# Optimization experiments

Measured on AMD Instinct MI355X. Metric: run time of the kernel, lower is better.

The kernel has to match this reference:

```python
import jax, jax.numpy as jnp
import numpy as np

D_MODEL = 1024
N_HEADS = 16
TOP_FACTOR = 5


def setup_inputs() -> dict:
    key = jax.random.key(0)
    ks = jax.random.split(key, 9)
    B, L, D = 2, 4096, D_MODEL
    s = 0.02
    return {
        "x": jax.random.normal(ks[0], (B, L, D), dtype=jnp.float32),
        "Wq": jax.random.normal(ks[1], (D, D), dtype=jnp.float32) * s,
        "bq": jnp.zeros((D,), dtype=jnp.float32),
        "Wk": jax.random.normal(ks[2], (D, D), dtype=jnp.float32) * s,
        "bk": jnp.zeros((D,), dtype=jnp.float32),
        "Wv": jax.random.normal(ks[3], (D, D), dtype=jnp.float32) * s,
        "bv": jnp.zeros((D,), dtype=jnp.float32),
        "Wo": jax.random.normal(ks[4], (D, D), dtype=jnp.float32) * s,
        "bo": jnp.zeros((D,), dtype=jnp.float32),
    }


def reference(x, Wq, bq, Wk, bk, Wv, bv, Wo, bo):
    B, L, D = x.shape
    H = N_HEADS
    hd = D // H
    BH = B * H
    top_u = max(1, L // TOP_FACTOR)

    def proj(W, b):
        # [B,L,D] -> [B*H, L, hd] (matches view + transpose(1,2) in torch)
        y = x @ W.T + b
        return y.reshape(B, L, H, hd).transpose(0, 2, 1, 3).reshape(BH, L, hd)

    Q = proj(Wq, bq)
    K = proj(Wk, bk)
    V = proj(Wv, bv)

    # select top-u queries per (batch,head) by L2 norm
    query_norms = jnp.linalg.norm(Q, axis=2)              # [BH, L]
    _, top_idx = jax.lax.top_k(query_norms, top_u)        # [BH, top_u]
    Q_sel = jnp.take_along_axis(Q, top_idx[:, :, None], axis=1)  # [BH, u, hd]

    scale = 1.0 / (hd ** 0.5)
    scores = jnp.einsum('bud,bld->bul', Q_sel, K) * scale  # [BH, u, L]
    attn = jax.nn.softmax(scores, axis=-1)
    out_sel = jnp.einsum('bul,bld->bud', attn, V)          # [BH, u, hd]

    # scatter selected outputs back; non-selected rows stay zero
    out_full = jnp.zeros((BH, L, hd), dtype=x.dtype)
    out_full = out_full.at[jnp.arange(BH)[:, None], top_idx].set(out_sel)

    out = out_full.reshape(B, H, L, hd).transpose(0, 2, 1, 3).reshape(B, L, D)
    return out @ Wo.T + bo
```

## Files before the change

kernel.cpp:

```cpp
#include <hip/hip_runtime.h>
#include <cstddef>
#include <cstdint>

constexpr int LSEQ = 4096;
constexpr int DM   = 1024;
constexpr int HD   = 64;
constexpr int BHT  = 32;
constexpr int TOPU = 819;
constexpr int MROWS = 8192;

typedef unsigned short u16;
typedef __attribute__((ext_vector_type(8))) short short8v;
typedef __attribute__((ext_vector_type(4))) short short4v;
typedef __attribute__((ext_vector_type(4))) float f32x4;

__device__ __forceinline__ u16 f2bf(float f) {
  uint32_t u = __float_as_uint(f);
  u += 0x7fffu + ((u >> 16) & 1u);
  return (u16)(u >> 16);
}
__device__ __forceinline__ float bf2f(u16 h) {
  return __uint_as_float(((uint32_t)h) << 16);
}

__device__ __forceinline__ void gl16(const void* g, void* l) {
  __builtin_amdgcn_global_load_lds(
      (const __attribute__((address_space(1))) void*)g,
      (__attribute__((address_space(3))) void*)l, 16, 0, 0);
}

__device__ __forceinline__ void inv_swz(int S, int& R, int& C) {
  const int R0 = ((S >> 5) ^ (S >> 7)) & 1;
  const int R1 = (S >> 6) & 1;
  R = ((S >> 6) << 1) | R0;
  C = (((S >> 3) & 1) ^ R0) | ((((S >> 4) & 1) ^ R1) << 1);
}

__device__ __forceinline__ void split3_body(const float* src, u16* p1, u16* p2,
                                            u16* p3, int i) {
  const float4 a = *reinterpret_cast<const float4*>(src + (size_t)i * 8);
  const float4 b = *reinterpret_cast<const float4*>(src + (size_t)i * 8 + 4);
  float e[8] = {a.x, a.y, a.z, a.w, b.x, b.y, b.z, b.w};
  short8v v1, v2, v3;
  #pragma unroll
  for (int j = 0; j < 8; ++j) {
    u16 h1 = f2bf(e[j]);        float r1 = e[j] - bf2f(h1);
    u16 h2 = f2bf(r1);          float r2 = r1 - bf2f(h2);
    u16 h3 = f2bf(r2);
    v1[j] = (short)h1; v2[j] = (short)h2; v3[j] = (short)h3;
  }
  *reinterpret_cast<short8v*>(p1 + (size_t)i * 8) = v1;
  *reinterpret_cast<short8v*>(p2 + (size_t)i * 8) = v2;
  *reinterpret_cast<short8v*>(p3 + (size_t)i * 8) = v3;
}

__device__ __forceinline__ void conv_body(const float* src, u16* dst, int i) {
  const float4 a = *reinterpret_cast<const float4*>(src + (size_t)i * 8);
  const float4 b = *reinterpret_cast<const float4*>(src + (size_t)i * 8 + 4);
  short8v v;
  v[0] = (short)f2bf(a.x); v[1] = (short)f2bf(a.y);
  v[2] = (short)f2bf(a.z); v[3] = (short)f2bf(a.w);
  v[4] = (short)f2bf(b.x); v[5] = (short)f2bf(b.y);
  v[6] = (short)f2bf(b.z); v[7] = (short)f2bf(b.w);
  *reinterpret_cast<short8v*>(dst + (size_t)i * 8) = v;
}

__global__ __launch_bounds__(256) void prep_all(
    const float* __restrict__ x,  const float* __restrict__ Wq,
    const float* __restrict__ Wk, const float* __restrict__ Wv,
    const float* __restrict__ Wo,
    u16* __restrict__ x1, u16* __restrict__ x2, u16* __restrict__ x3,
    u16* __restrict__ wq1, u16* __restrict__ wq2, u16* __restrict__ wq3,
    u16* __restrict__ Wkb, u16* __restrict__ Wvb, u16* __restrict__ Wob)
{
  const int NX = MROWS * DM / 8;
  const int NW = DM * DM / 8;
  int i = blockIdx.x * 256 + threadIdx.x;
  if (i < NX)                { split3_body(x,  x1,  x2,  x3,  i); return; }
  i -= NX;
  if (i < NW)                { split3_body(Wq, wq1, wq2, wq3, i); return; }
  i -= NW;
  if (i < NW)                { conv_body(Wk, Wkb, i); return; }
  i -= NW;
  if (i < NW)                { conv_body(Wv, Wvb, i); return; }
  i -= NW;
  if (i < NW)                { conv_body(Wo, Wob, i); }
}

__global__ __launch_bounds__(256) void gemm_q_split(
    const u16* __restrict__ X1, const u16* __restrict__ X2, const u16* __restrict__ X3,
    const u16* __restrict__ W1, const u16* __restrict__ W2, const u16* __restrict__ W3,
    const float* __restrict__ bias, float* __restrict__ Y,
    float* __restrict__ norms)
{
  __shared__ u16 As[3][128 * 32];
  __shared__ u16 Bs[3][128 * 32];
  const int tid = threadIdx.x;
  const int m0 = blockIdx.x * 128, n0 = blockIdx.y * 128;
  const int wid = tid >> 6, lane = tid & 63;
  const int wr = (wid >> 1) * 64, wc = (wid & 1) * 64;
  const int c = lane & 15, G = lane >> 4;

  int Rr[2], Cr[2];
  #pragma unroll
  for (int rr = 0; rr < 2; ++rr) inv_swz((tid + rr * 256) * 8, Rr[rr], Cr[rr]);

  f32x4 acc[4][4];
  #pragma unroll
  for (int mt = 0; mt < 4; ++mt)
    #pragma unroll
    for (int nt = 0; nt < 4; ++nt)
      acc[mt][nt] = (f32x4){0.f, 0.f, 0.f, 0.f};

  for (int k0 = 0; k0 < DM; k0 += 32) {
    #pragma unroll
    for (int rr = 0; rr < 2; ++rr) {
      const size_t goA = (size_t)(m0 + Rr[rr]) * DM + k0 + Cr[rr] * 8;
      const size_t goB = (size_t)(n0 + Rr[rr]) * DM + k0 + Cr[rr] * 8;
      const int lb = wid * 512 + rr * 2048;
      gl16(X1 + goA, &As[0][lb]);
      gl16(X2 + goA, &As[1][lb]);
      gl16(X3 + goA, &As[2][lb]);
      gl16(W1 + goB, &Bs[0][lb]);
      gl16(W2 + goB, &Bs[1][lb]);
      gl16(W3 + goB, &Bs[2][lb]);
    }
    __syncthreads();

    short8v bf[3][4];
    #pragma unroll
    for (int nt = 0; nt < 4; ++nt) {
      const int n = wc + nt * 16 + c;
      const int eo = (n * 32 + G * 8) ^ ((n & 7) << 3);
      bf[0][nt] = *reinterpret_cast<const short8v*>(&Bs[0][eo]);
      bf[1][nt] = *reinterpret_cast<const short8v*>(&Bs[1][eo]);
      bf[2][nt] = *reinterpret_cast<const short8v*>(&Bs[2][eo]);
    }
    #pragma unroll
    for (int mt = 0; mt < 4; ++mt) {
      const int m = wr + mt * 16 + c;
      const int eo = (m * 32 + G * 8) ^ ((m & 7) << 3);
      short8v a1 = *reinterpret_cast<const short8v*>(&As[0][eo]);
      short8v a2 = *reinterpret_cast<const short8v*>(&As[1][eo]);
      short8v a3 = *reinterpret_cast<const short8v*>(&As[2][eo]);
      #pragma unroll
      for (int nt = 0; nt < 4; ++nt) {
        acc[mt][nt] = __builtin_amdgcn_mfma_f32_16x16x32_bf16(a1, bf[0][nt], acc[mt][nt], 0, 0, 0);
        acc[mt][nt] = __builtin_amdgcn_mfma_f32_16x16x32_bf16(a1, bf[1][nt], acc[mt][nt], 0, 0, 0);
        acc[mt][nt] = __builtin_amdgcn_mfma_f32_16x16x32_bf16(a2, bf[0][nt], acc[mt][nt], 0, 0, 0);
        acc[mt][nt] = __builtin_amdgcn_mfma_f32_16x16x32_bf16(a2, bf[1][nt], acc[mt][nt], 0, 0, 0);
        acc[mt][nt] = __builtin_amdgcn_mfma_f32_16x16x32_bf16(a1, bf[2][nt], acc[mt][nt], 0, 0, 0);
        acc[mt][nt] = __builtin_amdgcn_mfma_f32_16x16x32_bf16(a3, bf[0][nt], acc[mt][nt], 0, 0, 0);
      }
    }
    __syncthreads();
  }

  float bb[4];
  #pragma unroll
  for (int nt = 0; nt < 4; ++nt) bb[nt] = bias[n0 + wc + nt * 16 + c];

  float ns[4][4];
  #pragma unroll
  for (int mt = 0; mt < 4; ++mt)
    #pragma unroll
    for (int r = 0; r < 4; ++r) ns[mt][r] = 0.f;

  #pragma unroll
  for (int mt = 0; mt < 4; ++mt) {
    #pragma unroll
    for (int nt = 0; nt < 4; ++nt) {
      const int n = n0 + wc + nt * 16 + c;
      const int h = n >> 6, d = n & 63;
      #pragma unroll
      for (int r = 0; r < 4; ++r) {
        const int m = m0 + wr + mt * 16 + G * 4 + r;
        const int b = m >> 12, l = m & (LSEQ - 1);
        const float val = acc[mt][nt][r] + bb[nt];
        Y[((size_t)((b << 4) + h) * LSEQ + l) * HD + d] = val;
        ns[mt][r] = fmaf(val, val, ns[mt][r]);
      }
    }
  }
  #pragma unroll
  for (int mt = 0; mt < 4; ++mt)
    #pragma unroll
    for (int r = 0; r < 4; ++r) {
      float v = ns[mt][r];
      v += __shfl_xor(v, 1); v += __shfl_xor(v, 2);
      v += __shfl_xor(v, 4); v += __shfl_xor(v, 8);
      ns[mt][r] = v;
    }
  if (c == 0) {
    const int h = (n0 + wc) >> 6;
    #pragma unroll
    for (int mt = 0; mt < 4; ++mt)
      #pragma unroll
      for (int r = 0; r < 4; ++r) {
        const int m = m0 + wr + mt * 16 + G * 4 + r;
        const int b = m >> 12, l = m & (LSEQ - 1);
        norms[(((size_t)((b << 4) + h)) << 12) + l] = ns[mt][r];
      }
  }
}

__global__ __launch_bounds__(256) void gemm_kv(
    const u16* __restrict__ Xb, const u16* __restrict__ Wkb, const u16* __restrict__ Wvb,
    const float* __restrict__ bkp, const float* __restrict__ bvp,
    u16* __restrict__ Kb, u16* __restrict__ VgT)
{
  __shared__ u16 smem[128 * 136];
  u16* As = smem;
  u16* Bs = smem + 4096;
  const int tid = threadIdx.x;
  const bool isV = blockIdx.y >= 8;
  const int m0 = blockIdx.x * 128, n0 = (blockIdx.y & 7) * 128;
  const u16* Wb = isV ? Wvb : Wkb;
  const float* bias = isV ? bvp : bkp;
  const int wid = tid >> 6, lane = tid & 63;
  const int wr = (wid >> 1) * 64, wc = (wid & 1) * 64;
  const int c = lane & 15, G = lane >> 4;

  int Rr[2], Cr[2];
  #pragma unroll
  for (int rr = 0; rr < 2; ++rr) inv_swz((tid + rr * 256) * 8, Rr[rr], Cr[rr]);

  f32x4 acc[4][4];
  #pragma unroll
  for (int mt = 0; mt < 4; ++mt)
    #pragma unroll
    for (int nt = 0; nt < 4; ++nt)
      acc[mt][nt] = (f32x4){0.f, 0.f, 0.f, 0.f};

  for (int k0 = 0; k0 < DM; k0 += 32) {
    #pragma unroll
    for (int rr = 0; rr < 2; ++rr) {
      const size_t goA = (size_t)(m0 + Rr[rr]) * DM + k0 + Cr[rr] * 8;
      const size_t goB = (size_t)(n0 + Rr[rr]) * DM + k0 + Cr[rr] * 8;
      const int lb = wid * 512 + rr * 2048;
      gl16(Xb + goA, As + lb);
      gl16(Wb + goB, Bs + lb);
    }
    __syncthreads();

    short8v af[4], bf[4];
    #pragma unroll
    for (int mt = 0; mt < 4; ++mt) {
      const int m = wr + mt * 16 + c;
      af[mt] = *reinterpret_cast<const short8v*>(As + ((m * 32 + G * 8) ^ ((m & 7) << 3)));
      const int n = wc + mt * 16 + c;
      bf[mt] = *reinterpret_cast<const short8v*>(Bs + ((n * 32 + G * 8) ^ ((n & 7) << 3)));
    }
    #pragma unroll
    for (int mt = 0; mt < 4; ++mt)
      #pragma unroll
      for (int nt = 0; nt < 4; ++nt)
        acc[mt][nt] = __builtin_amdgcn_mfma_f32_16x16x32_bf16(af[mt], bf[nt], acc[mt][nt], 0, 0, 0);
    __syncthreads();
  }

  float bb[4];
  #pragma unroll
  for (int nt = 0; nt < 4; ++nt) bb[nt] = bias[n0 + wc + nt * 16 + c];

  if (isV) {
    #pragma unroll
    for (int mt = 0; mt < 4; ++mt) {
      #pragma unroll
      for (int nt = 0; nt < 4; ++nt) {
        const int n = wc + nt * 16 + c;
        const int mloc = wr + mt * 16 + G * 4;
        short4v pv;
        #pragma unroll
        for (int r = 0; r < 4; ++r) pv[r] = (short)f2bf(acc[mt][nt][r] + bb[nt]);
        *reinterpret_cast<short4v*>(smem + n * 136 + mloc) = pv;
      }
    }
    __syncthreads();
    const int bb2 = m0 >> 12;
    const int ml0 = m0 & (LSEQ - 1);
    #pragma unroll
    for (int uu = 0; uu < 8; ++uu) {
      const int u = uu * 256 + tid;
      const int n = u >> 4, kg = u & 15;
      short8v vvv = *reinterpret_cast<const short8v*>(smem + n * 136 + kg * 8);
      const int h = (n0 + n) >> 6, d = (n0 + n) & 63;
      *reinterpret_cast<short8v*>(
          VgT + ((size_t)((bb2 << 4) + h) * HD + d) * LSEQ + ml0 + kg * 8) = vvv;
    }
  } else {
    #pragma unroll
    for (int mt = 0; mt < 4; ++mt) {
      #pragma unroll
      for (int nt = 0; nt < 4; ++nt) {
        const int n = n0 + wc + nt * 16 + c;
        const int h = n >> 6, d = n & 63;
        #pragma unroll
        for (int r = 0; r < 4; ++r) {
          const int m = m0 + wr + mt * 16 + G * 4 + r;
          const int b = m >> 12, l = m & (LSEQ - 1);
          Kb[((size_t)((b << 4) + h) * LSEQ + l) * HD + d] = f2bf(acc[mt][nt][r] + bb[nt]);
        }
      }
    }
  }
}

__global__ __launch_bounds__(256) void gemm_out(
    const u16* __restrict__ Xb, const u16* __restrict__ Wb,
    const float* __restrict__ bias, float* __restrict__ Y)
{
  __shared__ u16 As[128 * 32];
  __shared__ u16 Bs[128 * 32];
  const int tid = threadIdx.x;
  const int m0 = blockIdx.x * 128, n0 = blockIdx.y * 128;
  const int wid = tid >> 6, lane = tid & 63;
  const int wr = (wid >> 1) * 64, wc = (wid & 1) * 64;
  const int c = lane & 15, G = lane >> 4;

  int Rr[2], Cr[2];
  #pragma unroll
  for (int rr = 0; rr < 2; ++rr) inv_swz((tid + rr * 256) * 8, Rr[rr], Cr[rr]);

  f32x4 acc[4][4];
  #pragma unroll
  for (int mt = 0; mt < 4; ++mt)
    #pragma unroll
    for (int nt = 0; nt < 4; ++nt)
      acc[mt][nt] = (f32x4){0.f, 0.f, 0.f, 0.f};

  for (int k0 = 0; k0 < DM; k0 += 32) {
    #pragma unroll
    for (int rr = 0; rr < 2; ++rr) {
      const size_t goA = (size_t)(m0 + Rr[rr]) * DM + k0 + Cr[rr] * 8;
      const size_t goB = (size_t)(n0 + Rr[rr]) * DM + k0 + Cr[rr] * 8;
      const int lb = wid * 512 + rr * 2048;
      gl16(Xb + goA, As + lb);
      gl16(Wb + goB, Bs + lb);
    }
    __syncthreads();

    short8v af[4], bf[4];
    #pragma unroll
    for (int mt = 0; mt < 4; ++mt) {
      const int m = wr + mt * 16 + c;
      af[mt] = *reinterpret_cast<const short8v*>(As + ((m * 32 + G * 8) ^ ((m & 7) << 3)));
      const int n = wc + mt * 16 + c;
      bf[mt] = *reinterpret_cast<const short8v*>(Bs + ((n * 32 + G * 8) ^ ((n & 7) << 3)));
    }
    #pragma unroll
    for (int mt = 0; mt < 4; ++mt)
      #pragma unroll
      for (int nt = 0; nt < 4; ++nt)
        acc[mt][nt] = __builtin_amdgcn_mfma_f32_16x16x32_bf16(af[mt], bf[nt], acc[mt][nt], 0, 0, 0);
    __syncthreads();
  }

  float bb[4];
  #pragma unroll
  for (int nt = 0; nt < 4; ++nt) bb[nt] = bias[n0 + wc + nt * 16 + c];

  #pragma unroll
  for (int mt = 0; mt < 4; ++mt) {
    #pragma unroll
    for (int nt = 0; nt < 4; ++nt) {
      const int n = n0 + wc + nt * 16 + c;
      #pragma unroll
      for (int r = 0; r < 4; ++r) {
        const int m = m0 + wr + mt * 16 + G * 4 + r;
        Y[(size_t)m * DM + n] = acc[mt][nt][r] + bb[nt];
      }
    }
  }
}

__global__ __launch_bounds__(1024) void select_topk(
    const float* __restrict__ norms, int* __restrict__ top_idx)
{
  __shared__ unsigned int keys[LSEQ];
  __shared__ unsigned int hist[256];
  __shared__ unsigned int wsums[16];
  __shared__ unsigned int sh_b, sh_above;

  const int tid = threadIdx.x;
  const int bh = blockIdx.x;

  for (int l = tid; l < LSEQ; l += 1024)
    keys[l] = __float_as_uint(norms[bh * LSEQ + l]);
  __syncthreads();

  unsigned int prefix = 0, rem = TOPU, total_gt = 0;
  for (int shift = 24; shift >= 0; shift -= 8) {
    if (tid < 256) hist[tid] = 0;
    __syncthreads();
    for (int l = tid; l < LSEQ; l += 1024) {
      const unsigned int k = keys[l];
      const bool in = (shift == 24) || ((k >> (shift + 8)) == prefix);
      if (in) atomicAdd(&hist[(k >> shift) & 255], 1);
    }
    __syncthreads();
    if (tid == 0) {
      unsigned int cum = 0; int b = 255;
      for (; b > 0; --b) {
        const unsigned int h = hist[b];
        if (cum + h >= rem) break;
        cum += h;
      }
      sh_b = (unsigned int)b; sh_above = cum;
    }
    __syncthreads();
    prefix = (prefix << 8) | sh_b;
    total_gt += sh_above;
    rem -= sh_above;
    __syncthreads();
  }
  const unsigned int T = prefix;

  const int lane = tid & 63, wv = tid >> 6;
  const int l0 = tid * 4;

  {
    unsigned int flags = 0; int cnt = 0;
    #pragma unroll
    for (int j = 0; j < 4; ++j)
      if (keys[l0 + j] > T) { flags |= 1u << j; ++cnt; }
    int incl = cnt;
    #pragma unroll
    for (int off = 1; off < 64; off <<= 1) {
      int nv = __shfl_up(incl, off);
      if (lane >= off) incl += nv;
    }
    if (lane == 63) wsums[wv] = (unsigned int)incl;
    __syncthreads();
    if (tid == 0) {
      unsigned int run = 0;
      for (int w = 0; w < 16; ++w) { unsigned int t = wsums[w]; wsums[w] = run; run += t; }
    }
    __syncthreads();
    unsigned int pos = wsums[wv] + (unsigned int)(incl - cnt);
    #pragma unroll
    for (int j = 0; j < 4; ++j)
      if (flags & (1u << j)) top_idx[bh * TOPU + (pos++)] = l0 + j;
  }
  __syncthreads();

  {
    unsigned int flags = 0; int cnt = 0;
    #pragma unroll
    for (int j = 0; j < 4; ++j)
      if (keys[l0 + j] == T) { flags |= 1u << j; ++cnt; }
    int incl = cnt;
    #pragma unroll
    for (int off = 1; off < 64; off <<= 1) {
      int nv = __shfl_up(incl, off);
      if (lane >= off) incl += nv;
    }
    if (lane == 63) wsums[wv] = (unsigned int)incl;
    __syncthreads();
    if (tid == 0) {
      unsigned int run = 0;
      for (int w = 0; w < 16; ++w) { unsigned int t = wsums[w]; wsums[w] = run; run += t; }
    }
    __syncthreads();
    unsigned int r0 = wsums[wv] + (unsigned int)(incl - cnt);
    #pragma unroll
    for (int j = 0; j < 4; ++j)
      if (flags & (1u << j)) {
        if (r0 < rem) top_idx[bh * TOPU + total_gt + r0] = l0 + j;
        ++r0;
      }
  }
}

__global__ __launch_bounds__(256) void attn_mfma(
    const float* __restrict__ Qf, const u16* __restrict__ Kg,
    const u16* __restrict__ VgT, const int* __restrict__ tix,
    float* __restrict__ Opart, float* __restrict__ MLpart)
{
  __shared__ u16 Kc[128 * 64];
  __shared__ u16 Vt[64 * 128];
  __shared__ u16 Pt[4][16 * 136];

  const int tid = threadIdx.x;
  const int wid = tid >> 6, lane = tid & 63;
  const int c = lane & 15, G = lane >> 4;

  const int l = blockIdx.x;
  const int grp = l >> 3;
  const int bh = (grp / 26) * 8 + (l & 7);
  const int rem = grp % 26;
  const int qb = rem >> 1, ks = rem & 1;

  const size_t bhL = (size_t)bh * LSEQ;
  const int rglob = qb * 64 + wid * 16 + c;
  const int rowidx = (rglob < TOPU) ? tix[bh * TOPU + rglob] : -1;

  short8v qf[2];
  #pragma unroll
  for (int kf = 0; kf < 2; ++kf) {
    if (rowidx >= 0) {
      const float* qp = Qf + (bhL + rowidx) * HD + kf * 32 + G * 8;
      const float4 x0 = *reinterpret_cast<const float4*>(qp);
      const float4 x1 = *reinterpret_cast<const float4*>(qp + 4);
      short8v v;
      v[0] = (short)f2bf(x0.x * 0.125f); v[1] = (short)f2bf(x0.y * 0.125f);
      v[2] = (short)f2bf(x0.z * 0.125f); v[3] = (short)f2bf(x0.w * 0.125f);
      v[4] = (short)f2bf(x1.x * 0.125f); v[5] = (short)f2bf(x1.y * 0.125f);
      v[6] = (short)f2bf(x1.z * 0.125f); v[7] = (short)f2bf(x1.w * 0.125f);
      qf[kf] = v;
    } else {
      short8v v;
      #pragma unroll
      for (int j = 0; j < 8; ++j) v[j] = 0;
      qf[kf] = v;
    }
  }

  float m = -1e30f, lsum = 0.f;
  f32x4 oacc[4];
  #pragma unroll
  for (int dt = 0; dt < 4; ++dt) oacc[dt] = (f32x4){0.f, 0.f, 0.f, 0.f};

  const int ko0 = ks * (LSEQ / 2);
  const int wbase = (tid & ~63) * 8;
  for (int t = 0; t < LSEQ / 256; ++t) {
    const int ko = ko0 + t * 128;
    #pragma unroll
    for (int uu = 0; uu < 4; ++uu) {
      const int S = (uu * 256 + tid) * 8;
      const int key = S >> 6, dgk = ((S >> 3) & 7) ^ (key & 7);
      gl16(Kg + (bhL + ko + key) * HD + dgk * 8, Kc + uu * 2048 + wbase);
      const int d = S >> 7, kgv = ((S >> 3) & 15) ^ (d & 7);
      gl16(VgT + ((size_t)bh * HD + d) * LSEQ + ko + kgv * 8, Vt + uu * 2048 + wbase);
    }
    __syncthreads();

    f32x4 sacc[8];
    __builtin_amdgcn_s_setprio(1);
    #pragma unroll
    for (int kt = 0; kt < 8; ++kt) {
      const int key = kt * 16 + c;
      short8v kb0 = *reinterpret_cast<const short8v*>(
          Kc + key * 64 + (((0 + G) ^ (key & 7)) << 3));
      short8v kb1 = *reinterpret_cast<const short8v*>(
          Kc + key * 64 + (((4 + G) ^ (key & 7)) << 3));
      f32x4 s = (f32x4){0.f, 0.f, 0.f, 0.f};
      s = __builtin_amdgcn_mfma_f32_16x16x32_bf16(kb0, qf[0], s, 0, 0, 0);
      s = __builtin_amdgcn_mfma_f32_16x16x32_bf16(kb1, qf[1], s, 0, 0, 0);
      sacc[kt] = s;
    }
    __builtin_amdgcn_s_setprio(0);

    float smax = -1e30f;
    #pragma unroll
    for (int kt = 0; kt < 8; ++kt) {
      float a0 = fmaxf(sacc[kt][0], sacc[kt][1]);
      float a1 = fmaxf(sacc[kt][2], sacc[kt][3]);
      smax = fmaxf(smax, fmaxf(a0, a1));
    }
    smax = fmaxf(smax, __shfl_xor(smax, 16));
    smax = fmaxf(smax, __shfl_xor(smax, 32));
    const float mnew = fmaxf(m, smax);
    const float corr = __expf(m - mnew);
    float ssum = 0.f;
    #pragma unroll
    for (int kt = 0; kt < 8; ++kt) {
      float p0 = __expf(sacc[kt][0] - mnew);
      float p1 = __expf(sacc[kt][1] - mnew);
      float p2 = __expf(sacc[kt][2] - mnew);
      float p3 = __expf(sacc[kt][3] - mnew);
      ssum += (p0 + p1) + (p2 + p3);
      short4v pv;
      pv[0] = (short)f2bf(p0); pv[1] = (short)f2bf(p1);
      pv[2] = (short)f2bf(p2); pv[3] = (short)f2bf(p3);
      *reinterpret_cast<short4v*>(&Pt[wid][c * 136 + kt * 16 + G * 4]) = pv;
    }
    ssum += __shfl_xor(ssum, 16);
    ssum += __shfl_xor(ssum, 32);
    lsum = lsum * corr + ssum;
    m = mnew;
    #pragma unroll
    for (int dt = 0; dt < 4; ++dt) oacc[dt] *= corr;

    __builtin_amdgcn_s_setprio(1);
    #pragma unroll
    for (int kf = 0; kf < 4; ++kf) {
      short8v pf = *reinterpret_cast<const short8v*>(
          &Pt[wid][c * 136 + kf * 32 + G * 8]);
      #pragma unroll
      for (int dt = 0; dt < 4; ++dt) {
        const int d = dt * 16 + c;
        short8v vf = *reinterpret_cast<const short8v*>(
            Vt + d * 128 + (((kf * 4 + G) ^ (d & 7)) << 3));
        oacc[dt] = __builtin_amdgcn_mfma_f32_16x16x32_bf16(vf, pf, oacc[dt], 0, 0, 0);
      }
    }
    __builtin_amdgcn_s_setprio(0);
    __syncthreads();
  }

  const int q = wid * 16 + c;
  const size_t pb = ((size_t)(bh * 13 + qb) * 2 + ks) * 64 + q;
  float* op = Opart + pb * 64;
  #pragma unroll
  for (int dt = 0; dt < 4; ++dt)
    *reinterpret_cast<f32x4*>(op + dt * 16 + G * 4) = oacc[dt];
  if (G == 0) {
    MLpart[pb * 2]     = m;
    MLpart[pb * 2 + 1] = lsum;
  }
}

__global__ __launch_bounds__(256) void attn_combine(
    const float* __restrict__ Opart, const float* __restrict__ MLpart,
    const int* __restrict__ tix, u16* __restrict__ O1b)
{
  const int bq = blockIdx.x;
  const int bh = bq / 13, qb = bq % 13;
  const int tid = threadIdx.x;
  const int q = tid >> 2, dq = (tid & 3) * 16;
  const int rglob = qb * 64 + q;
  if (rglob >= TOPU) return;
  const int rowidx = tix[bh * TOPU + rglob];

  const size_t p0 = ((size_t)bq * 2 + 0) * 64 + q;
  const size_t p1 = ((size_t)bq * 2 + 1) * 64 + q;
  const float m0 = MLpart[p0 * 2], l0 = MLpart[p0 * 2 + 1];
  const float m1 = MLpart[p1 * 2], l1 = MLpart[p1 * 2 + 1];
  const float mx = fmaxf(m0, m1);
  const float c0 = __expf(m0 - mx), c1 = __expf(m1 - mx);
  const float linv = 1.0f / (l0 * c0 + l1 * c1);

  const int b = bh >> 4, h = bh & 15;
  u16* dst = O1b + (size_t)(b * LSEQ + rowidx) * DM + h * HD + dq;
  const float* o0 = Opart + p0 * 64 + dq;
  const float* o1 = Opart + p1 * 64 + dq;
  #pragma unroll
  for (int i = 0; i < 16; i += 4) {
    float4 a  = *reinterpret_cast<const float4*>(o0 + i);
    float4 bb = *reinterpret_cast<const float4*>(o1 + i);
    short4v o;
    o[0] = (short)f2bf((a.x * c0 + bb.x * c1) * linv);
    o[1] = (short)f2bf((a.y * c0 + bb.y * c1) * linv);
    o[2] = (short)f2bf((a.z * c0 + bb.z * c1) * linv);
    o[3] = (short)f2bf((a.w * c0 + bb.w * c1) * linv);
    *reinterpret_cast<short4v*>(dst + i) = o;
  }
}

extern "C" void kernel_launch(void* const* d_in, const int* in_sizes, int n_in,
                              void* d_out, int out_size, void* d_ws, size_t ws_size,
                              hipStream_t stream) {
  const float* x  = (const float*)d_in[0];
  const float* Wq = (const float*)d_in[1];
  const float* bq = (const float*)d_in[2];
  const float* Wk = (const float*)d_in[3];
  const float* bk = (const float*)d_in[4];
  const float* Wv = (const float*)d_in[5];
  const float* bv = (const float*)d_in[6];
  const float* Wo = (const float*)d_in[7];
  const float* bo = (const float*)d_in[8];
  float* out = (float*)d_out;

  char* w = (char*)d_ws;
  float* Qb = (float*)w;  w += (size_t)BHT * LSEQ * HD * 4;
  u16* x1   = (u16*)w;    w += (size_t)MROWS * DM * 2;
  u16* x2   = (u16*)w;    w += (size_t)MROWS * DM * 2;
  u16* x3   = (u16*)w;    w += (size_t)MROWS * DM * 2;
  u16* VgT  = (u16*)w;    w += (size_t)BHT * HD * LSEQ * 2;
  u16* Wkb  = (u16*)w;    w += (size_t)DM * DM * 2;
  u16* Wvb  = (u16*)w;    w += (size_t)DM * DM * 2;
  u16* Wob  = (u16*)w;    w += (size_t)DM * DM * 2;
  u16* wq1  = (u16*)w;    w += (size_t)DM * DM * 2;
  u16* wq2  = (u16*)w;    w += (size_t)DM * DM * 2;
  u16* wq3  = (u16*)w;    w += (size_t)DM * DM * 2;
  float* norms = (float*)w; w += (size_t)BHT * LSEQ * 4;

  u16*   O1b  = x2;
  u16*   Kb   = x3;
  int*   tix  = (int*)wq2;
  float* Opart  = (float*)x1;
  float* MLpart = Opart + (size_t)832 * 64 * 64;

  prep_all<<<6144, 256, 0, stream>>>(x, Wq, Wk, Wv, Wo,
                                     x1, x2, x3, wq1, wq2, wq3, Wkb, Wvb, Wob);

  gemm_q_split<<<dim3(MROWS / 128, DM / 128), 256, 0, stream>>>(
      x1, x2, x3, wq1, wq2, wq3, bq, Qb, norms);

  gemm_kv<<<dim3(MROWS / 128, 16), 256, 0, stream>>>(x1, Wkb, Wvb, bk, bv, Kb, VgT);

  select_topk<<<BHT, 1024, 0, stream>>>(norms, tix);

  hipMemsetAsync(O1b, 0, (size_t)MROWS * DM * 2, stream);

  attn_mfma<<<832, 256, 0, stream>>>(Qb, Kb, VgT, tix, Opart, MLpart);
  attn_combine<<<416, 256, 0, stream>>>(Opart, MLpart, tix, O1b);

  gemm_out<<<dim3(MROWS / 128, DM / 128), 256, 0, stream>>>(O1b, Wob, bo, out);
}
```

Before: 303.5 us.

## Replace 3-way bf16 split Q projection with 2-way scaled fp16 split

The Q projection, which must be near-fp32 accurate so top-k query selection matches, previously used a three-term bf16 split needing six MFMAs per tile step and three operand planes per input. It now splits x and Wq into an fp16 high part plus an fp16 residual scaled by 256. It uses three f16 MFMAs into two accumulators and rescales the cross terms in the epilogue. This removes half the MFMA work and one third of the LDS and global traffic for this GEMM. The costs are fp16 range limits and slightly different error behaviour, which could change top-k ties, and the prep kernel must also write a separate bf16 copy of x for the K/V GEMM.

Measured after the change: 310.0 us. 2.1% more time.

```diff
diff --git a/kernel.cpp b/kernel.cpp
--- a/kernel.cpp
+++ b/kernel.cpp
@@ -12,6 +12,7 @@
 typedef unsigned short u16;
 typedef __attribute__((ext_vector_type(8))) short short8v;
 typedef __attribute__((ext_vector_type(4))) short short4v;
+typedef __attribute__((ext_vector_type(8))) _Float16 half8v;
 typedef __attribute__((ext_vector_type(4))) float f32x4;
 
 __device__ __forceinline__ u16 f2bf(float f) {
@@ -36,22 +37,42 @@
   C = (((S >> 3) & 1) ^ R0) | ((((S >> 4) & 1) ^ R1) << 1);
 }
 
-__device__ __forceinline__ void split3_body(const float* src, u16* p1, u16* p2,
-                                            u16* p3, int i) {
+__device__ __forceinline__ void splitx_body(const float* src, u16* p1, u16* p2,
+                                            u16* pb, int i) {
   const float4 a = *reinterpret_cast<const float4*>(src + (size_t)i * 8);
   const float4 b = *reinterpret_cast<const float4*>(src + (size_t)i * 8 + 4);
   float e[8] = {a.x, a.y, a.z, a.w, b.x, b.y, b.z, b.w};
-  short8v v1, v2, v3;
+  short8v v1, v2, vb;
   #pragma unroll
   for (int j = 0; j < 8; ++j) {
-    u16 h1 = f2bf(e[j]);        float r1 = e[j] - bf2f(h1);
-    u16 h2 = f2bf(r1);          float r2 = r1 - bf2f(h2);
-    u16 h3 = f2bf(r2);
-    v1[j] = (short)h1; v2[j] = (short)h2; v3[j] = (short)h3;
+    _Float16 h1 = (_Float16)e[j];
+    float r = e[j] - (float)h1;
+    _Float16 h2 = (_Float16)(r * 256.0f);
+    v1[j] = __builtin_bit_cast(short, h1);
+    v2[j] = __builtin_bit_cast(short, h2);
+    vb[j] = (short)f2bf(e[j]);
   }
   *reinterpret_cast<short8v*>(p1 + (size_t)i * 8) = v1;
   *reinterpret_cast<short8v*>(p2 + (size_t)i * 8) = v2;
-  *reinterpret_cast<short8v*>(p3 + (size_t)i * 8) = v3;
+  *reinterpret_cast<short8v*>(pb + (size_t)i * 8) = vb;
+}
+
+__device__ __forceinline__ void split2h_body(const float* src, u16* p1, u16* p2,
+                                             int i) {
+  const float4 a = *reinterpret_cast<const float4*>(src + (size_t)i * 8);
+  const float4 b = *reinterpret_cast<const float4*>(src + (size_t)i * 8 + 4);
+  float e[8] = {a.x, a.y, a.z, a.w, b.x, b.y, b.z, b.w};
+  short8v v1, v2;
+  #pragma unroll
+  for (int j = 0; j < 8; ++j) {
+    _Float16 h1 = (_Float16)e[j];
+    float r = e[j] - (float)h1;
+    _Float16 h2 = (_Float16)(r * 256.0f);
+    v1[j] = __builtin_bit_cast(short, h1);
+    v2[j] = __builtin_bit_cast(short, h2);
+  }
+  *reinterpret_cast<short8v*>(p1 + (size_t)i * 8) = v1;
+  *reinterpret_cast<short8v*>(p2 + (size_t)i * 8) = v2;
 }
 
 __device__ __forceinline__ void conv_body(const float* src, u16* dst, int i) {
@@ -69,32 +90,32 @@
     const float* __restrict__ x,  const float* __restrict__ Wq,
     const float* __restrict__ Wk, const float* __restrict__ Wv,
     const float* __restrict__ Wo,
-    u16* __restrict__ x1, u16* __restrict__ x2, u16* __restrict__ x3,
-    u16* __restrict__ wq1, u16* __restrict__ wq2, u16* __restrict__ wq3,
+    u16* __restrict__ xh1, u16* __restrict__ xh2, u16* __restrict__ x1b,
+    u16* __restrict__ wqh1, u16* __restrict__ wqh2,
     u16* __restrict__ Wkb, u16* __restrict__ Wvb, u16* __restrict__ Wob)
 {
   const int NX = MROWS * DM / 8;
   const int NW = DM * DM / 8;
   int i = blockIdx.x * 256 + threadIdx.x;
-  if (i < NX)                { split3_body(x,  x1,  x2,  x3,  i); return; }
+  if (i < NX)  { splitx_body(x, xh1, xh2, x1b, i); return; }
   i -= NX;
-  if (i < NW)                { split3_body(Wq, wq1, wq2, wq3, i); return; }
+  if (i < NW)  { split2h_body(Wq, wqh1, wqh2, i); return; }
   i -= NW;
-  if (i < NW)                { conv_body(Wk, Wkb, i); return; }
+  if (i < NW)  { conv_body(Wk, Wkb, i); return; }
   i -= NW;
-  if (i < NW)                { conv_body(Wv, Wvb, i); return; }
+  if (i < NW)  { conv_body(Wv, Wvb, i); return; }
   i -= NW;
-  if (i < NW)                { conv_body(Wo, Wob, i); }
+  if (i < NW)  { conv_body(Wo, Wob, i); }
 }
 
 __global__ __launch_bounds__(256) void gemm_q_split(
-    const u16* __restrict__ X1, const u16* __restrict__ X2, const u16* __restrict__ X3,
-    const u16* __restrict__ W1, const u16* __restrict__ W2, const u16* __restrict__ W3,
+    const u16* __restrict__ X1, const u16* __restrict__ X2,
+    const u16* __restrict__ W1, const u16* __restrict__ W2,
     const float* __restrict__ bias, float* __restrict__ Y,
     float* __restrict__ norms)
 {
-  __shared__ u16 As[3][128 * 32];
-  __shared__ u16 Bs[3][128 * 32];
+  __shared__ u16 As[2][128 * 32];
+  __shared__ u16 Bs[2][128 * 32];
   const int tid = threadIdx.x;
   const int m0 = blockIdx.x * 128, n0 = blockIdx.y * 128;
   const int wid = tid >> 6, lane = tid & 63;
@@ -105,12 +126,14 @@
   #pragma unroll
   for (int rr = 0; rr < 2; ++rr) inv_swz((tid + rr * 256) * 8, Rr[rr], Cr[rr]);
 
-  f32x4 acc[4][4];
+  f32x4 acc0[4][4], acc1[4][4];
   #pragma unroll
   for (int mt = 0; mt < 4; ++mt)
     #pragma unroll
-    for (int nt = 0; nt < 4; ++nt)
-      acc[mt][nt] = (f32x4){0.f, 0.f, 0.f, 0.f};
+    for (int nt = 0; nt < 4; ++nt) {
+      acc0[mt][nt] = (f32x4){0.f, 0.f, 0.f, 0.f};
+      acc1[mt][nt] = (f32x4){0.f, 0.f, 0.f, 0.f};
+    }
 
   for (int k0 = 0; k0 < DM; k0 += 32) {
     #pragma unroll
@@ -120,37 +143,30 @@
       const int lb = wid * 512 + rr * 2048;
       gl16(X1 + goA, &As[0][lb]);
       gl16(X2 + goA, &As[1][lb]);
-      gl16(X3 + goA, &As[2][lb]);
       gl16(W1 + goB, &Bs[0][lb]);
       gl16(W2 + goB, &Bs[1][lb]);
-      gl16(W3 + goB, &Bs[2][lb]);
-    }
-    __syncthreads();
-
-    short8v bf[3][4];
+    }
+    __syncthreads();
+
+    half8v bf1[4], bf2[4];
     #pragma unroll
     for (int nt = 0; nt < 4; ++nt) {
       const int n = wc + nt * 16 + c;
       const int eo = (n * 32 + G * 8) ^ ((n & 7) << 3);
-      bf[0][nt] = *reinterpret_cast<const short8v*>(&Bs[0][eo]);
-      bf[1][nt] = *reinterpret_cast<const short8v*>(&Bs[1][eo]);
-      bf[2][nt] = *reinterpret_cast<const short8v*>(&Bs[2][eo]);
+      bf1[nt] = *reinterpret_cast<const half8v*>(&Bs[0][eo]);
+      bf2[nt] = *reinterpret_cast<const half8v*>(&Bs[1][eo]);
     }
     #pragma unroll
     for (int mt = 0; mt < 4; ++mt) {
       const int m = wr + mt * 16 + c;
       const int eo = (m * 32 + G * 8) ^ ((m & 7) << 3);
-      short8v a1 = *reinterpret_cast<const short8v*>(&As[0][eo]);
-      short8v a2 = *reinterpret_cast<const short8v*>(&As[1][eo]);
-      short8v a3 = *reinterpret_cast<const short8v*>(&As[2][eo]);
+      half8v a1 = *reinterpret_cast<const half8v*>(&As[0][eo]);
+      half8v a2 = *reinterpret_cast<const half8v*>(&As[1][eo]);
       #pragma unroll
       for (int nt = 0; nt < 4; ++nt) {
-        acc[mt][nt] = __builtin_amdgcn_mfma_f32_16x16x32_bf16(a1, bf[0][nt], acc[mt][nt], 0, 0, 0);
-        acc[mt][nt] = __builtin_amdgcn_mfma_f32_16x16x32_bf16(a1, bf[1][nt], acc[mt][nt], 0, 0, 0);
-        acc[mt][nt] = __builtin_amdgcn_mfma_f32_16x16x32_bf16(a2, bf[0][nt], acc[mt][nt], 0, 0, 0);
-        acc[mt][nt] = __builtin_amdgcn_mfma_f32_16x16x32_bf16(a2, bf[1][nt], acc[mt][nt], 0, 0, 0);
-        acc[mt][nt] = __builtin_amdgcn_mfma_f32_16x16x32_bf16(a1, bf[2][nt], acc[mt][nt], 0, 0, 0);
-        acc[mt][nt] = __builtin_amdgcn_mfma_f32_16x16x32_bf16(a3, bf[0][nt], acc[mt][nt], 0, 0, 0);
+        acc0[mt][nt] = __builtin_amdgcn_mfma_f32_16x16x32_f16(a1, bf1[nt], acc0[mt][nt], 0, 0, 0);
+        acc1[mt][nt] = __builtin_amdgcn_mfma_f32_16x16x32_f16(a1, bf2[nt], acc1[mt][nt], 0, 0, 0);
+        acc1[mt][nt] = __builtin_amdgcn_mfma_f32_16x16x32_f16(a2, bf1[nt], acc1[mt][nt], 0, 0, 0);
       }
     }
     __syncthreads();
@@ -166,6 +182,7 @@
     #pragma unroll
     for (int r = 0; r < 4; ++r) ns[mt][r] = 0.f;
 
+  constexpr float INV256 = 1.0f / 256.0f;
   #pragma unroll
   for (int mt = 0; mt < 4; ++mt) {
     #pragma unroll
@@ -176,7 +193,7 @@
       for (int r = 0; r < 4; ++r) {
         const int m = m0 + wr + mt * 16 + G * 4 + r;
         const int b = m >> 12, l = m & (LSEQ - 1);
-        const float val = acc[mt][nt][r] + bb[nt];
+        const float val = acc0[mt][nt][r] + acc1[mt][nt][r] * INV256 + bb[nt];
         Y[((size_t)((b << 4) + h) * LSEQ + l) * HD + d] = val;
         ns[mt][r] = fmaf(val, val, ns[mt][r]);
       }
@@ -664,31 +681,30 @@
 
   char* w = (char*)d_ws;
   float* Qb = (float*)w;  w += (size_t)BHT * LSEQ * HD * 4;
-  u16* x1   = (u16*)w;    w += (size_t)MROWS * DM * 2;
-  u16* x2   = (u16*)w;    w += (size_t)MROWS * DM * 2;
-  u16* x3   = (u16*)w;    w += (size_t)MROWS * DM * 2;
+  u16* xh1  = (u16*)w;    w += (size_t)MROWS * DM * 2;
+  u16* xh2  = (u16*)w;    w += (size_t)MROWS * DM * 2;
+  u16* x1b  = (u16*)w;    w += (size_t)MROWS * DM * 2;
   u16* VgT  = (u16*)w;    w += (size_t)BHT * HD * LSEQ * 2;
   u16* Wkb  = (u16*)w;    w += (size_t)DM * DM * 2;
   u16* Wvb  = (u16*)w;    w += (size_t)DM * DM * 2;
   u16* Wob  = (u16*)w;    w += (size_t)DM * DM * 2;
-  u16* wq1  = (u16*)w;    w += (size_t)DM * DM * 2;
-  u16* wq2  = (u16*)w;    w += (size_t)DM * DM * 2;
-  u16* wq3  = (u16*)w;    w += (size_t)DM * DM * 2;
+  u16* wqh1 = (u16*)w;    w += (size_t)DM * DM * 2;
+  u16* wqh2 = (u16*)w;    w += (size_t)DM * DM * 2;
   float* norms = (float*)w; w += (size_t)BHT * LSEQ * 4;
 
-  u16*   O1b  = x2;
-  u16*   Kb   = x3;
-  int*   tix  = (int*)wq2;
-  float* Opart  = (float*)x1;
+  u16*   O1b  = xh1;
+  u16*   Kb   = xh2;
+  int*   tix  = (int*)wqh2;
+  float* Opart  = (float*)x1b;
   float* MLpart = Opart + (size_t)832 * 64 * 64;
 
   prep_all<<<6144, 256, 0, stream>>>(x, Wq, Wk, Wv, Wo,
-                                     x1, x2, x3, wq1, wq2, wq3, Wkb, Wvb, Wob);
+                                     xh1, xh2, x1b, wqh1, wqh2, Wkb, Wvb, Wob);
 
   gemm_q_split<<<dim3(MROWS / 128, DM / 128), 256, 0, stream>>>(
-      x1, x2, x3, wq1, wq2, wq3, bq, Qb, norms);
-
-  gemm_kv<<<dim3(MROWS / 128, 16), 256, 0, stream>>>(x1, Wkb, Wvb, bk, bv, Kb, VgT);
+      xh1, xh2, wqh1, wqh2, bq, Qb, norms);
+
+  gemm_kv<<<dim3(MROWS / 128, 16), 256, 0, stream>>>(x1b, Wkb, Wvb, bk, bv, Kb, VgT);
 
   select_topk<<<BHT, 1024, 0, stream>>>(norms, tix);
 
```

## Fuse Q, K and V projection GEMMs into one launch with separate K buffer

Applied to the files above, without the earlier changes.

Merges the split-precision Q projection and the K/V projection GEMMs into a single kernel whose grid y-dimension selects Q, V or K tiles. This removes a launch boundary and tail idle time between the two GEMMs, so all three projections can run concurrently. When the workspace is large enough, K gets its own buffer instead of reusing x3, which the Q GEMM still reads. Otherwise it falls back to two launches that run K after Q. The shared-memory allocation grows to the Q kernel's size for all blocks, which may lower occupancy for the K/V tiles.

New measurement: 297.0 us. -2.1%, faster.

```diff
diff --git a/kernel.cpp b/kernel.cpp
--- a/kernel.cpp
+++ b/kernel.cpp
@@ -76,27 +76,28 @@
   const int NX = MROWS * DM / 8;
   const int NW = DM * DM / 8;
   int i = blockIdx.x * 256 + threadIdx.x;
-  if (i < NX)                { split3_body(x,  x1,  x2,  x3,  i); return; }
+  if (i < NX)  { split3_body(x,  x1,  x2,  x3,  i); return; }
   i -= NX;
-  if (i < NW)                { split3_body(Wq, wq1, wq2, wq3, i); return; }
+  if (i < NW)  { split3_body(Wq, wq1, wq2, wq3, i); return; }
   i -= NW;
-  if (i < NW)                { conv_body(Wk, Wkb, i); return; }
+  if (i < NW)  { conv_body(Wk, Wkb, i); return; }
   i -= NW;
-  if (i < NW)                { conv_body(Wv, Wvb, i); return; }
+  if (i < NW)  { conv_body(Wv, Wvb, i); return; }
   i -= NW;
-  if (i < NW)                { conv_body(Wo, Wob, i); }
-}
-
-__global__ __launch_bounds__(256) void gemm_q_split(
+  if (i < NW)  { conv_body(Wo, Wob, i); }
+}
+
+__device__ __forceinline__ void proj_q_body(
+    u16* smem,
     const u16* __restrict__ X1, const u16* __restrict__ X2, const u16* __restrict__ X3,
     const u16* __restrict__ W1, const u16* __restrict__ W2, const u16* __restrict__ W3,
     const float* __restrict__ bias, float* __restrict__ Y,
-    float* __restrict__ norms)
+    float* __restrict__ norms, int bx, int ny)
 {
-  __shared__ u16 As[3][128 * 32];
-  __shared__ u16 Bs[3][128 * 32];
+  u16* As[3] = {smem, smem + 4096, smem + 8192};
+  u16* Bs[3] = {smem + 12288, smem + 16384, smem + 20480};
   const int tid = threadIdx.x;
-  const int m0 = blockIdx.x * 128, n0 = blockIdx.y * 128;
+  const int m0 = bx * 128, n0 = ny * 128;
   const int wid = tid >> 6, lane = tid & 63;
   const int wr = (wid >> 1) * 64, wc = (wid & 1) * 64;
   const int c = lane & 15, G = lane >> 4;
@@ -118,12 +119,12 @@
       const size_t goA = (size_t)(m0 + Rr[rr]) * DM + k0 + Cr[rr] * 8;
       const size_t goB = (size_t)(n0 + Rr[rr]) * DM + k0 + Cr[rr] * 8;
       const int lb = wid * 512 + rr * 2048;
-      gl16(X1 + goA, &As[0][lb]);
-      gl16(X2 + goA, &As[1][lb]);
-      gl16(X3 + goA, &As[2][lb]);
-      gl16(W1 + goB, &Bs[0][lb]);
-      gl16(W2 + goB, &Bs[1][lb]);
-      gl16(W3 + goB, &Bs[2][lb]);
+      gl16(X1 + goA, As[0] + lb);
+      gl16(X2 + goA, As[1] + lb);
+      gl16(X3 + goA, As[2] + lb);
+      gl16(W1 + goB, Bs[0] + lb);
+      gl16(W2 + goB, Bs[1] + lb);
+      gl16(W3 + goB, Bs[2] + lb);
     }
     __syncthreads();
 
@@ -132,17 +133,17 @@
     for (int nt = 0; nt < 4; ++nt) {
       const int n = wc + nt * 16 + c;
       const int eo = (n * 32 + G * 8) ^ ((n & 7) << 3);
-      bf[0][nt] = *reinterpret_cast<const short8v*>(&Bs[0][eo]);
-      bf[1][nt] = *reinterpret_cast<const short8v*>(&Bs[1][eo]);
-      bf[2][nt] = *reinterpret_cast<const short8v*>(&Bs[2][eo]);
+      bf[0][nt] = *reinterpret_cast<const short8v*>(Bs[0] + eo);
+      bf[1][nt] = *reinterpret_cast<const short8v*>(Bs[1] + eo);
+      bf[2][nt] = *reinterpret_cast<const short8v*>(Bs[2] + eo);
     }
     #pragma unroll
     for (int mt = 0; mt < 4; ++mt) {
       const int m = wr + mt * 16 + c;
       const int eo = (m * 32 + G * 8) ^ ((m & 7) << 3);
-      short8v a1 = *reinterpret_cast<const short8v*>(&As[0][eo]);
-      short8v a2 = *reinterpret_cast<const short8v*>(&As[1][eo]);
-      short8v a3 = *reinterpret_cast<const short8v*>(&As[2][eo]);
+      short8v a1 = *reinterpret_cast<const short8v*>(As[0] + eo);
+      short8v a2 = *reinterpret_cast<const short8v*>(As[1] + eo);
+      short8v a3 = *reinterpret_cast<const short8v*>(As[2] + eo);
       #pragma unroll
       for (int nt = 0; nt < 4; ++nt) {
         acc[mt][nt] = __builtin_amdgcn_mfma_f32_16x16x32_bf16(a1, bf[0][nt], acc[mt][nt], 0, 0, 0);
@@ -204,19 +205,15 @@
   }
 }
 
-__global__ __launch_bounds__(256) void gemm_kv(
-    const u16* __restrict__ Xb, const u16* __restrict__ Wkb, const u16* __restrict__ Wvb,
-    const float* __restrict__ bkp, const float* __restrict__ bvp,
-    u16* __restrict__ Kb, u16* __restrict__ VgT)
+__device__ __forceinline__ void proj_kv_body(
+    u16* smem, const u16* __restrict__ Xb, const u16* __restrict__ Wb,
+    const float* __restrict__ bias, u16* __restrict__ Kb, u16* __restrict__ VgT,
+    bool isV, int bx, int ny)
 {
-  __shared__ u16 smem[128 * 136];
   u16* As = smem;
   u16* Bs = smem + 4096;
   const int tid = threadIdx.x;
-  const bool isV = blockIdx.y >= 8;
-  const int m0 = blockIdx.x * 128, n0 = (blockIdx.y & 7) * 128;
-  const u16* Wb = isV ? Wvb : Wkb;
-  const float* bias = isV ? bvp : bkp;
+  const int m0 = bx * 128, n0 = ny * 128;
   const int wid = tid >> 6, lane = tid & 63;
   const int wr = (wid >> 1) * 64, wc = (wid & 1) * 64;
   const int c = lane & 15, G = lane >> 4;
@@ -303,6 +300,26 @@
         }
       }
     }
+  }
+}
+
+__global__ __launch_bounds__(256) void gemm_proj(
+    const u16* __restrict__ X1, const u16* __restrict__ X2, const u16* __restrict__ X3,
+    const u16* __restrict__ W1, const u16* __restrict__ W2, const u16* __restrict__ W3,
+    const u16* __restrict__ Wkb, const u16* __restrict__ Wvb,
+    const float* __restrict__ bq, const float* __restrict__ bk, const float* __restrict__ bv,
+    float* __restrict__ Qb, float* __restrict__ norms,
+    u16* __restrict__ Kb, u16* __restrict__ VgT, int y_off)
+{
+  __shared__ u16 smem[24576];
+  const int by = blockIdx.y + y_off;
+  const int bx = blockIdx.x;
+  if (by < 8) {
+    proj_q_body(smem, X1, X2, X3, W1, W2, W3, bq, Qb, norms, bx, by);
+  } else if (by < 16) {
+    proj_kv_body(smem, X1, Wvb, bv, Kb, VgT, true, bx, by - 8);
+  } else {
+    proj_kv_body(smem, X1, Wkb, bk, Kb, VgT, false, bx, by - 16);
   }
 }
 
@@ -675,9 +692,12 @@
   u16* wq2  = (u16*)w;    w += (size_t)DM * DM * 2;
   u16* wq3  = (u16*)w;    w += (size_t)DM * DM * 2;
   float* norms = (float*)w; w += (size_t)BHT * LSEQ * 4;
+  u16* Kb_ext = (u16*)w;  w += (size_t)BHT * LSEQ * HD * 2;
+
+  const bool fusedK = ws_size >= (size_t)(w - (char*)d_ws);
+  u16* Kb = fusedK ? Kb_ext : x3;
 
   u16*   O1b  = x2;
-  u16*   Kb   = x3;
   int*   tix  = (int*)wq2;
   float* Opart  = (float*)x1;
   float* MLpart = Opart + (size_t)832 * 64 * 64;
@@ -685,10 +705,15 @@
   prep_all<<<6144, 256, 0, stream>>>(x, Wq, Wk, Wv, Wo,
                                      x1, x2, x3, wq1, wq2, wq3, Wkb, Wvb, Wob);
 
-  gemm_q_split<<<dim3(MROWS / 128, DM / 128), 256, 0, stream>>>(
-      x1, x2, x3, wq1, wq2, wq3, bq, Qb, norms);
-
-  gemm_kv<<<dim3(MROWS / 128, 16), 256, 0, stream>>>(x1, Wkb, Wvb, bk, bv, Kb, VgT);
+  if (fusedK) {
+    gemm_proj<<<dim3(64, 24), 256, 0, stream>>>(
+        x1, x2, x3, wq1, wq2, wq3, Wkb, Wvb, bq, bk, bv, Qb, norms, Kb, VgT, 0);
+  } else {
+    gemm_proj<<<dim3(64, 16), 256, 0, stream>>>(
+        x1, x2, x3, wq1, wq2, wq3, Wkb, Wvb, bq, bk, bv, Qb, norms, Kb, VgT, 0);
+    gemm_proj<<<dim3(64, 8), 256, 0, stream>>>(
+        x1, x2, x3, wq1, wq2, wq3, Wkb, Wvb, bq, bk, bv, Qb, norms, Kb, VgT, 16);
+  }
 
   select_topk<<<BHT, 1024, 0, stream>>>(norms, tix);
 
```
